# Kernel optimization log

Hardware: AMD Instinct MI355X
Metric: run time of the kernel (lower is better)

The kernel has to match this reference:

```python
import jax, jax.numpy as jnp
import numpy as np

EPS = 1e-12  # matches torch.nn.functional.normalize default eps


def _l2norm_ch(x):
    # normalize over channel axis (dim=1), x: [B, D, N]
    n = jnp.sqrt(jnp.sum(x * x, axis=1, keepdims=True))
    return x / jnp.maximum(n, EPS)


def setup_inputs() -> dict:
    key = jax.random.key(0)
    k0, k1, kq, kk, kv = jax.random.split(key, 5)
    B, D, H, W = 8, 128, 64, 64
    return {
        "vol0": jax.random.normal(k0, (B, D, H, W), dtype=jnp.float32),
        "vol1": jax.random.normal(k1, (B, D, H, W), dtype=jnp.float32),
        "Wq": jax.random.normal(kq, (D, D), dtype=jnp.float32) * 0.05,
        "Wk": jax.random.normal(kk, (D, D), dtype=jnp.float32) * 0.05,
        "Wv": jax.random.normal(kv, (D, D), dtype=jnp.float32) * 0.05,
    }


def reference(vol0, vol1, Wq, Wk, Wv):
    B, D, H, W = vol0.shape
    N = H * W
    x0 = vol0.reshape(B, D, N)
    x1 = vol1.reshape(B, D, N)

    # 1x1 convs (bias=False) == channel matmuls; residual connections enabled
    q = jnp.einsum('od,bdn->bon', Wq, x0) + x0
    k = jnp.einsum('od,bdn->bon', Wk, x1) + x1
    v0 = jnp.einsum('od,bdn->bon', Wv, x0) + x0
    v1 = jnp.einsum('od,bdn->bon', Wv, x1) + x1

    # normalise dot product: L2-normalize over channel dim
    q = _l2norm_ch(q)
    k = _l2norm_ch(k)

    # correlation volume + row softmax: cvolume[b, n, m]
    cvolume = jax.nn.softmax(jnp.einsum('bdn,bdm->bnm', q, k), axis=2)

    # warp v1 by attention: v1w[b, d, n] = sum_m v1[b, d, m] * cvolume[b, n, m]
    v1w = jnp.einsum('bdm,bnm->bdn', v1, cvolume)

    # position encoder (meshgrid with 'ij' indexing, as legacy torch.meshgrid)
    u = jnp.linspace(-1.0, 1.0, H)
    v = jnp.linspace(-1.0, 1.0, W)
    uu, vv = jnp.meshgrid(u, v, indexing='ij')
    grid = jnp.stack([uu, vv], axis=0).reshape(2, N)  # [2, N]
    pos = jnp.einsum('cm,bnm->bcn', grid, cvolume)  # [B, 2, N]

    # max-score channel: [B, 1, N]
    max_score = jnp.max(cvolume, axis=2)[:, None, :]

    agg = jnp.concatenate([v0, v1w, pos, max_score], axis=1)  # [B, 2D+3, N]
    return agg.reshape(B, 2 * D + 3, H, W)
```

## Files before the change

kernel.cpp:

```cpp
#include <hip/hip_runtime.h>
#include <hip/hip_bf16.h>

#define B_   8
#define D_   128
#define N_   4096
#define CH   259

typedef short bf8 __attribute__((ext_vector_type(8)));
typedef float f4  __attribute__((ext_vector_type(4)));

typedef unsigned int as1_u32 __attribute__((address_space(1)));
typedef unsigned int as3_u32 __attribute__((address_space(3)));

__device__ __forceinline__ void gll16(const void* g, void* l) {
    __builtin_amdgcn_global_load_lds((as1_u32*)(unsigned long long)g,
                                     (as3_u32*)(unsigned int)(unsigned long long)l,
                                     16, 0, 0);
}

__device__ __forceinline__ unsigned short f2bf(float x) {
    unsigned int u = __float_as_uint(x);
    return (unsigned short)((u + 0x7FFFu + ((u >> 16) & 1u)) >> 16);
}

__device__ __forceinline__ unsigned int cvtpk(float lo, float hi) {
    unsigned int r;
    asm("v_cvt_pk_bf16_f32 %0, %1, %2" : "=v"(r) : "v"(lo), "v"(hi));
    return r;
}

__global__ void wconv_kernel(const float* __restrict__ Wq,
                             const float* __restrict__ Wk,
                             const float* __restrict__ Wv,
                             unsigned short* __restrict__ Wb) {
    const float* src = (blockIdx.x == 0) ? Wq : (blockIdx.x == 1) ? Wk : Wv;
    unsigned short* dst = Wb + (size_t)blockIdx.x * D_ * D_;
    for (int i = threadIdx.x; i < D_ * D_; i += blockDim.x) dst[i] = f2bf(src[i]);
}

__global__ __launch_bounds__(256, 2) void proj_kernel(
    const float* __restrict__ vol0, const float* __restrict__ vol1,
    const unsigned short* __restrict__ Wb, float* __restrict__ out,
    unsigned short* __restrict__ Qp, unsigned short* __restrict__ Kh,
    unsigned short* __restrict__ V1T)
{
    __shared__ __align__(16) float xs[2][D_ * 64];

    const int tid  = threadIdx.x;
    const int wave = tid >> 6, lane = tid & 63;
    const int l15  = lane & 15, lh = lane >> 4;

    const int bid = blockIdx.x;
    const int swz = (bid & 7) * 64 + (bid >> 3);
    const int b   = swz >> 6;
    const int n0  = (swz & 63) * 64;

    #pragma unroll
    for (int a = 0; a < 2; ++a) {
        const char* src = (const char*)((a ? vol1 : vol0) + (size_t)b * D_ * N_ + n0);
        char* dstb = (char*)&xs[a][0];
        #pragma unroll
        for (int i = 0; i < 8; ++i) {
            int dst16 = i * 4096 + tid * 16;
            int row = dst16 >> 8, cb = dst16 & 255;
            gll16(src + (size_t)row * (N_ * 4) + (cb ^ (((row >> 3) & 7) << 4)), dstb + dst16);
        }
    }
    __syncthreads();

    const int nrow = wave * 16 + l15;

    auto afrag = [&](const float* base, int k) -> bf8 {
        const int dbase = k * 32 + lh * 8;
        const unsigned int cb = ((unsigned int)(nrow * 4)) ^ (((unsigned int)((k * 4 + lh) & 7)) << 4);
        const float* p = base + dbase * 64 + (cb >> 2);
        union { bf8 v; unsigned int w[4]; } u;
        #pragma unroll
        for (int jj = 0; jj < 4; ++jj)
            u.w[jj] = cvtpk(p[(2 * jj) * 64], p[(2 * jj + 1) * 64]);
        return u.v;
    };

    f4 aq[8], ak[8], a0v[8], a1v[8];
    #pragma unroll
    for (int ob = 0; ob < 8; ++ob) {
        aq[ob] = (f4){0.f,0.f,0.f,0.f}; ak[ob] = (f4){0.f,0.f,0.f,0.f};
        a0v[ob] = (f4){0.f,0.f,0.f,0.f}; a1v[ob] = (f4){0.f,0.f,0.f,0.f};
    }

    const unsigned short* Wqb = Wb;
    const unsigned short* Wkb = Wb + D_ * D_;
    const unsigned short* Wvb = Wb + 2 * D_ * D_;

    for (int k = 0; k < 4; ++k) {
        bf8 x0f = afrag(&xs[0][0], k);
        bf8 x1f = afrag(&xs[1][0], k);
        #pragma unroll
        for (int ob = 0; ob < 8; ++ob) {
            const size_t woff = ((size_t)(ob * 16 + l15)) * D_ + k * 32 + lh * 8;
            bf8 wq = *(const bf8*)(Wqb + woff);
            bf8 wk = *(const bf8*)(Wkb + woff);
            bf8 wv = *(const bf8*)(Wvb + woff);
            aq[ob]  = __builtin_amdgcn_mfma_f32_16x16x32_bf16(x0f, wq, aq[ob], 0, 0, 0);
            ak[ob]  = __builtin_amdgcn_mfma_f32_16x16x32_bf16(x1f, wk, ak[ob], 0, 0, 0);
            a0v[ob] = __builtin_amdgcn_mfma_f32_16x16x32_bf16(x0f, wv, a0v[ob], 0, 0, 0);
            a1v[ob] = __builtin_amdgcn_mfma_f32_16x16x32_bf16(x1f, wv, a1v[ob], 0, 0, 0);
        }
    }

    float ssq[4] = {0.f,0.f,0.f,0.f}, ssk[4] = {0.f,0.f,0.f,0.f};
    #pragma unroll
    for (int ob = 0; ob < 8; ++ob) {
        const int o = ob * 16 + l15;
        const unsigned int okey = (((unsigned int)((o >> 3) & 7)) << 4);
        #pragma unroll
        for (int r = 0; r < 4; ++r) {
            int n = wave * 16 + lh * 4 + r;
            int ci = o * 64 + (int)(((((unsigned int)(n * 4)) ^ okey) >> 2));
            float r0 = xs[0][ci], r1 = xs[1][ci];
            aq[ob][r] += r0; ak[ob][r] += r1; a0v[ob][r] += r0; a1v[ob][r] += r1;
            ssq[r] = fmaf(aq[ob][r], aq[ob][r], ssq[r]);
            ssk[r] = fmaf(ak[ob][r], ak[ob][r], ssk[r]);
        }
    }
    #pragma unroll
    for (int off = 1; off < 16; off <<= 1)
        #pragma unroll
        for (int r = 0; r < 4; ++r) {
            ssq[r] += __shfl_xor(ssq[r], off, 64);
            ssk[r] += __shfl_xor(ssk[r], off, 64);
        }
    float rq[4], rk[4];
    #pragma unroll
    for (int r = 0; r < 4; ++r) {
        rq[r] = 1.44269504088896f / fmaxf(sqrtf(ssq[r]), 1e-12f);
        rk[r] = 1.0f / fmaxf(sqrtf(ssk[r]), 1e-12f);
    }

    const int nbase = n0 + wave * 16 + lh * 4;
    #pragma unroll
    for (int ob = 0; ob < 8; ++ob) {
        const int o = ob * 16 + l15;
        *(f4*)(out + ((size_t)(b * CH + o)) * N_ + nbase) = a0v[ob];
        uint2 pv; pv.x = cvtpk(a1v[ob][0], a1v[ob][1]); pv.y = cvtpk(a1v[ob][2], a1v[ob][3]);
        *(uint2*)(V1T + ((size_t)(b * D_ + o)) * N_ + nbase) = pv;
        uint2 pq; pq.x = cvtpk(aq[ob][0]*rq[0], aq[ob][1]*rq[1]);
        pq.y = cvtpk(aq[ob][2]*rq[2], aq[ob][3]*rq[3]);
        *(uint2*)(Qp + ((size_t)(b * D_ + o)) * N_ + nbase) = pq;
    }

    __syncthreads();
    float* chunk = &xs[0][0] + wave * 2176;
    #pragma unroll
    for (int ob = 0; ob < 8; ++ob) {
        const int o = ob * 16 + l15;
        #pragma unroll
        for (int r = 0; r < 4; ++r) chunk[o * 17 + lh * 4 + r] = ak[ob][r] * rk[r];
    }
    asm volatile("s_waitcnt lgkmcnt(0)" ::: "memory");
    __builtin_amdgcn_sched_barrier(0);
    {
        const int o0 = (lane & 15) * 8, nr = lane >> 4;
        #pragma unroll
        for (int t = 0; t < 4; ++t) {
            int nl = t * 4 + nr;
            float f[8];
            #pragma unroll
            for (int j = 0; j < 8; ++j) f[j] = chunk[(o0 + j) * 17 + nl];
            uint4 st;
            st.x = cvtpk(f[0], f[1]); st.y = cvtpk(f[2], f[3]);
            st.z = cvtpk(f[4], f[5]); st.w = cvtpk(f[6], f[7]);
            *(uint4*)(Kh + ((size_t)(b * N_ + n0 + wave * 16 + nl)) * D_ + o0) = st;
        }
    }
}

__global__ __launch_bounds__(256, 2) void attn_kernel(
    const unsigned short* __restrict__ Qp, const unsigned short* __restrict__ Kh,
    const unsigned short* __restrict__ V1T, float* __restrict__ out)
{
    __shared__ __align__(16) char smem[73728];
    char* KB = smem;
    char* VB = smem + 32768;
    char* PB = smem + 65536;

    const int tid  = threadIdx.x;
    const int wave = tid >> 6, lane = tid & 63;
    const int l15  = lane & 15, lh = lane >> 4;
    const int mhalf = wave & 1, qpair = wave >> 1;

    const int bid = blockIdx.x;
    const int swz = (bid & 7) * 64 + (bid >> 3);
    const int b   = swz >> 6;
    const int n0  = (swz & 63) * 64;
    const int nw  = n0 + qpair * 32;

    bf8 qf[2][4];
    const unsigned short* Qb = Qp + (size_t)b * D_ * N_;
    #pragma unroll
    for (int qg = 0; qg < 2; ++qg)
        #pragma unroll
        for (int dc = 0; dc < 4; ++dc) {
            union { bf8 v; unsigned short e[8]; } u;
            #pragma unroll
            for (int j = 0; j < 8; ++j)
                u.e[j] = Qb[((size_t)(dc * 32 + lh * 8 + j)) * N_ + nw + qg * 16 + l15];
            qf[qg][dc] = u.v;
        }

    f4 acc[2][8];
    #pragma unroll
    for (int qg = 0; qg < 2; ++qg)
        #pragma unroll
        for (int dc = 0; dc < 8; ++dc) acc[qg][dc] = (f4){0.f,0.f,0.f,0.f};
    float lsum[2] = {0.f, 0.f}, pu[2] = {0.f, 0.f}, pvv[2] = {0.f, 0.f};
    float Mp[2] = {-1e30f, -1e30f};

    float vb0[8];
    #pragma unroll
    for (int s = 0; s < 2; ++s)
        #pragma unroll
        for (int r = 0; r < 4; ++r)
            vb0[s * 4 + r] = -1.f + (2.f / 63.f) * (float)(s * 16 + lh * 4 + r);

    const char* Kbytes = (const char*)(Kh + (size_t)b * N_ * D_);
    const char* Vbytes = (const char*)(V1T + (size_t)b * D_ * N_);
    char* Pw = PB + wave * 2048;

    unsigned int koffs[4], voffs[4];
    #pragma unroll
    for (int ii = 0; ii < 4; ++ii) {
        int r = wave * 16 + ii * 4 + (lane >> 4);
        unsigned int col = (unsigned int)((lane & 15) * 16);
        koffs[ii] = (unsigned int)(((r >> 5) * 2048 + (r & 31)) * 256)
                  + (col ^ (unsigned int)((r & 7) << 4));
        int vr = wave * 64 + ii * 16 + (lane >> 2);
        int ch = vr & 127;
        unsigned int mc = (unsigned int)((lane & 3) * 16);
        voffs[ii] = (unsigned int)(ch * 8192 + (vr >> 7) * 4096)
                  + (mc ^ (unsigned int)(((ch >> 1) & 3) << 4));
    }
    auto stage = [&](int buf, int t) {
        const char* ks = Kbytes + (size_t)t * 8192;
        char* kd = KB + buf * 16384 + wave * 4096;
        #pragma unroll
        for (int ii = 0; ii < 4; ++ii) gll16(ks + koffs[ii], kd + ii * 1024);
        const char* vs = Vbytes + (size_t)t * 64;
        char* vd = VB + buf * 16384 + wave * 4096;
        #pragma unroll
        for (int ii = 0; ii < 4; ++ii) gll16(vs + voffs[ii], vd + ii * 1024);
    };

    unsigned int kcol[4];
    #pragma unroll
    for (int dc = 0; dc < 4; ++dc)
        kcol[dc] = ((unsigned int)(dc * 64 + lh * 16)) ^ ((unsigned int)((l15 & 7) << 4));
    const unsigned int pkey  = ((unsigned int)((l15 >> 1) & 3)) << 4;
    const unsigned int prow0 = (unsigned int)(l15 * 64);
    const unsigned int prow1 = (unsigned int)((16 + l15) * 64);
    const unsigned int vx    = ((unsigned int)(lh * 16)) ^ pkey;

    stage(0, 0);
    __syncthreads();

    const float utb = -1.f + (2.f / 63.f) * (float)(mhalf * 32);

    for (int t = 0; t < 64; ++t) {
        const int cur = t & 1;
        if (t + 1 < 64) stage(cur ^ 1, t + 1);

        const char* Kc = KB + cur * 16384 + mhalf * 8192 + l15 * 256;
        const char* Vc = VB + cur * 16384 + mhalf * 8192 + l15 * 64;

        f4 s00 = (f4){0.f,0.f,0.f,0.f}, s01 = (f4){0.f,0.f,0.f,0.f};
        f4 s10 = (f4){0.f,0.f,0.f,0.f}, s11 = (f4){0.f,0.f,0.f,0.f};
        __builtin_amdgcn_s_setprio(1);
        #pragma unroll
        for (int dc = 0; dc < 4; ++dc) {
            bf8 k0 = *(const bf8*)(Kc + kcol[dc]);
            bf8 k1 = *(const bf8*)(Kc + 4096 + kcol[dc]);
            s00 = __builtin_amdgcn_mfma_f32_16x16x32_bf16(k0, qf[0][dc], s00, 0, 0, 0);
            s10 = __builtin_amdgcn_mfma_f32_16x16x32_bf16(k0, qf[1][dc], s10, 0, 0, 0);
            s01 = __builtin_amdgcn_mfma_f32_16x16x32_bf16(k1, qf[0][dc], s01, 0, 0, 0);
            s11 = __builtin_amdgcn_mfma_f32_16x16x32_bf16(k1, qf[1][dc], s11, 0, 0, 0);
        }
        __builtin_amdgcn_s_setprio(0);

        const float ut   = utb + (2.f / 63.f) * (float)(t >> 1);
        const float voff = (t & 1) ? (64.f / 63.f) : 0.f;
        #pragma unroll
        for (int qg = 0; qg < 2; ++qg) {
            f4 sa = qg ? s10 : s00, sb = qg ? s11 : s01;
            float p[8];
            #pragma unroll
            for (int r = 0; r < 4; ++r) {
                p[r]     = __builtin_amdgcn_exp2f(sa[r]);
                p[4 + r] = __builtin_amdgcn_exp2f(sb[r]);
            }
            Mp[qg] = fmaxf(Mp[qg], fmaxf(fmaxf(fmaxf(sa[0], sa[1]), fmaxf(sa[2], sa[3])),
                                         fmaxf(fmaxf(sb[0], sb[1]), fmaxf(sb[2], sb[3]))));
            float ps = ((p[0]+p[1]) + (p[2]+p[3])) + ((p[4]+p[5]) + (p[6]+p[7]));
            float pvp = 0.f;
            #pragma unroll
            for (int i = 0; i < 8; ++i) pvp = fmaf(vb0[i], p[i], pvp);
            lsum[qg] += ps;
            pu[qg]  = fmaf(ut, ps, pu[qg]);
            pvv[qg] = fmaf(voff, ps, pvv[qg] + pvp);
            const unsigned int pr = qg ? prow1 : prow0;
            uint2 w0; w0.x = cvtpk(p[0], p[1]); w0.y = cvtpk(p[2], p[3]);
            uint2 w1; w1.x = cvtpk(p[4], p[5]); w1.y = cvtpk(p[6], p[7]);
            *(uint2*)(Pw + pr + (((unsigned int)(lh * 8)) ^ pkey))      = w0;
            *(uint2*)(Pw + pr + (((unsigned int)(32 + lh * 8)) ^ pkey)) = w1;
        }
        asm volatile("s_waitcnt lgkmcnt(0)" ::: "memory");
        __builtin_amdgcn_sched_barrier(0);

        bf8 pf0 = *(const bf8*)(Pw + prow0 + vx);
        bf8 pf1 = *(const bf8*)(Pw + prow1 + vx);
        __builtin_amdgcn_s_setprio(1);
        #pragma unroll
        for (int dc = 0; dc < 8; ++dc) {
            bf8 vf = *(const bf8*)(Vc + dc * 1024 + vx);
            acc[0][dc] = __builtin_amdgcn_mfma_f32_16x16x32_bf16(pf0, vf, acc[0][dc], 0, 0, 0);
            acc[1][dc] = __builtin_amdgcn_mfma_f32_16x16x32_bf16(pf1, vf, acc[1][dc], 0, 0, 0);
        }
        __builtin_amdgcn_s_setprio(0);
        __syncthreads();
    }

    #pragma unroll
    for (int qg = 0; qg < 2; ++qg) {
        #pragma unroll
        for (int off = 16; off < 64; off <<= 1) {
            lsum[qg] += __shfl_xor(lsum[qg], off, 64);
            pu[qg]   += __shfl_xor(pu[qg], off, 64);
            pvv[qg]  += __shfl_xor(pvv[qg], off, 64);
            Mp[qg]    = fmaxf(Mp[qg], __shfl_xor(Mp[qg], off, 64));
        }
    }

    __syncthreads();
    float* ex  = (float*)smem;
    float* stt = (float*)(smem + 34816);
    if (lane < 16) {
        #pragma unroll
        for (int qg = 0; qg < 2; ++qg) {
            float* s = stt + ((wave * 2 + qg) * 16 + l15) * 4;
            s[0] = lsum[qg]; s[1] = pu[qg]; s[2] = pvv[qg]; s[3] = Mp[qg];
        }
    }
    #pragma unroll
    for (int qg = 0; qg < 2; ++qg)
        #pragma unroll
        for (int j = 0; j < 4; ++j) {
            float* e = ex + (((wave * 2 + qg) * 4 + j) * 16 + lh * 4) * 17 + l15;
            if (mhalf == 0) {
                #pragma unroll
                for (int r = 0; r < 4; ++r) e[r * 17] = acc[qg][4 + j][r];
            } else {
                #pragma unroll
                for (int r = 0; r < 4; ++r) e[r * 17] = acc[qg][j][r];
            }
        }
    __syncthreads();

    const int pw_ = wave ^ 1;
    float rl[2], PUm[2], PVm[2], Mm[2];
    #pragma unroll
    for (int qg = 0; qg < 2; ++qg) {
        const float* s = stt + ((pw_ * 2 + qg) * 16 + l15) * 4;
        float Lm = lsum[qg] + s[0];
        PUm[qg] = pu[qg]  + s[1];
        PVm[qg] = pvv[qg] + s[2];
        Mm[qg]  = fmaxf(Mp[qg], s[3]);
        rl[qg]  = __builtin_amdgcn_rcpf(Lm);
    }

    #pragma unroll
    for (int qg = 0; qg < 2; ++qg) {
        float rlr[4];
        #pragma unroll
        for (int r = 0; r < 4; ++r)
            rlr[r] = __shfl(rl[qg], (lane & 48) + lh * 4 + r, 64);
        #pragma unroll
        for (int j = 0; j < 4; ++j) {
            const float* e = ex + (((pw_ * 2 + qg) * 4 + j) * 16 + lh * 4) * 17 + l15;
            f4 v;
            if (mhalf == 0) {
                #pragma unroll
                for (int r = 0; r < 4; ++r) v[r] = (acc[qg][j][r] + e[r * 17]) * rlr[r];
            } else {
                #pragma unroll
                for (int r = 0; r < 4; ++r) v[r] = (acc[qg][4 + j][r] + e[r * 17]) * rlr[r];
            }
            const int och = 128 + (mhalf * 4 + j) * 16 + l15;
            *(f4*)(out + ((size_t)(b * CH + och)) * N_ + nw + qg * 16 + lh * 4) = v;
        }
    }
    if (mhalf == 0 && lh == 0) {
        #pragma unroll
        for (int qg = 0; qg < 2; ++qg) {
            const int gn = nw + qg * 16 + l15;
            out[((size_t)(b * CH + 256)) * N_ + gn] = PUm[qg] * rl[qg];
            out[((size_t)(b * CH + 257)) * N_ + gn] = PVm[qg] * rl[qg];
            out[((size_t)(b * CH + 258)) * N_ + gn] =
                __builtin_amdgcn_exp2f(Mm[qg]) * rl[qg];
        }
    }
}

extern "C" void kernel_launch(void* const* d_in, const int* in_sizes, int n_in,
                              void* d_out, int out_size, void* d_ws, size_t ws_size,
                              hipStream_t stream) {
    const float* vol0 = (const float*)d_in[0];
    const float* vol1 = (const float*)d_in[1];
    const float* Wq   = (const float*)d_in[2];
    const float* Wk   = (const float*)d_in[3];
    const float* Wv   = (const float*)d_in[4];
    float* out = (float*)d_out;

    char* ws = (char*)d_ws;
    const size_t QP_BYTES  = (size_t)B_ * D_ * N_ * 2;
    const size_t KH_BYTES  = (size_t)B_ * N_ * D_ * 2;
    const size_t V1T_BYTES = (size_t)B_ * D_ * N_ * 2;
    unsigned short* Qp  = (unsigned short*)(ws);
    unsigned short* Kh  = (unsigned short*)(ws + QP_BYTES);
    unsigned short* V1T = (unsigned short*)(ws + QP_BYTES + KH_BYTES);
    unsigned short* Wb  = (unsigned short*)(ws + QP_BYTES + KH_BYTES + V1T_BYTES);

    hipLaunchKernelGGL(wconv_kernel, dim3(3), dim3(256), 0, stream, Wq, Wk, Wv, Wb);
    hipLaunchKernelGGL(proj_kernel, dim3(512), dim3(256), 0, stream,
                       vol0, vol1, Wb, out, Qp, Kh, V1T);
    hipLaunchKernelGGL(attn_kernel, dim3(512), dim3(256), 0, stream,
                       Qp, Kh, V1T, out);
}
```

Measured before the change: 152.1 us.

## Load V fragments directly from global memory in a tiled layout, dropping the V LDS stage

The projection kernel now writes V1 in a chunked layout, so each attention wave can fetch its MFMA B-operand fragments for V straight from global memory as contiguous 16-byte loads. The V double buffer in LDS is removed, shrinking shared memory from 72KB to 40KB, and launch bounds are raised to allow 3 blocks per CU. The aim is less LDS traffic and higher occupancy. In exchange, global load latency is exposed inside the loop, since the loads are issued at the start of each iteration, and 8 bf8 fragments per iteration add register pressure.

```diff
diff --git a/kernel.cpp b/kernel.cpp
--- a/kernel.cpp
+++ b/kernel.cpp
@@ -42,7 +42,7 @@
     const float* __restrict__ vol0, const float* __restrict__ vol1,
     const unsigned short* __restrict__ Wb, float* __restrict__ out,
     unsigned short* __restrict__ Qp, unsigned short* __restrict__ Kh,
-    unsigned short* __restrict__ V1T)
+    unsigned short* __restrict__ V2)
 {
     __shared__ __align__(16) float xs[2][D_ * 64];
 
@@ -138,12 +138,17 @@
     }
 
     const int nbase = n0 + wave * 16 + lh * 4;
+    const int mh_ = nbase >> 11;
+    const int tt  = (nbase & 2047) >> 5;
+    const int ml  = nbase & 31;
+    char* v2chunk = (char*)V2 + (((size_t)(b * 2 + mh_) * 64 + tt) * 8192) + ml * 2;
+
     #pragma unroll
     for (int ob = 0; ob < 8; ++ob) {
         const int o = ob * 16 + l15;
         *(f4*)(out + ((size_t)(b * CH + o)) * N_ + nbase) = a0v[ob];
         uint2 pv; pv.x = cvtpk(a1v[ob][0], a1v[ob][1]); pv.y = cvtpk(a1v[ob][2], a1v[ob][3]);
-        *(uint2*)(V1T + ((size_t)(b * D_ + o)) * N_ + nbase) = pv;
+        *(uint2*)(v2chunk + (size_t)o * 64) = pv;
         uint2 pq; pq.x = cvtpk(aq[ob][0]*rq[0], aq[ob][1]*rq[1]);
         pq.y = cvtpk(aq[ob][2]*rq[2], aq[ob][3]*rq[3]);
         *(uint2*)(Qp + ((size_t)(b * D_ + o)) * N_ + nbase) = pq;
@@ -175,14 +180,13 @@
     }
 }
 
-__global__ __launch_bounds__(256, 2) void attn_kernel(
+__global__ __launch_bounds__(256, 3) void attn_kernel(
     const unsigned short* __restrict__ Qp, const unsigned short* __restrict__ Kh,
-    const unsigned short* __restrict__ V1T, float* __restrict__ out)
+    const unsigned short* __restrict__ V2, float* __restrict__ out)
 {
-    __shared__ __align__(16) char smem[73728];
+    __shared__ __align__(16) char smem[40960];
     char* KB = smem;
-    char* VB = smem + 32768;
-    char* PB = smem + 65536;
+    char* PB = smem + 32768;
 
     const int tid  = threadIdx.x;
     const int wave = tid >> 6, lane = tid & 63;
@@ -224,31 +228,23 @@
             vb0[s * 4 + r] = -1.f + (2.f / 63.f) * (float)(s * 16 + lh * 4 + r);
 
     const char* Kbytes = (const char*)(Kh + (size_t)b * N_ * D_);
-    const char* Vbytes = (const char*)(V1T + (size_t)b * D_ * N_);
+    const char* Vg = (const char*)V2 + ((size_t)(b * 2 + mhalf)) * 524288
+                   + l15 * 64 + lh * 16;
     char* Pw = PB + wave * 2048;
 
-    unsigned int koffs[4], voffs[4];
+    unsigned int koffs[4];
     #pragma unroll
     for (int ii = 0; ii < 4; ++ii) {
         int r = wave * 16 + ii * 4 + (lane >> 4);
         unsigned int col = (unsigned int)((lane & 15) * 16);
         koffs[ii] = (unsigned int)(((r >> 5) * 2048 + (r & 31)) * 256)
                   + (col ^ (unsigned int)((r & 7) << 4));
-        int vr = wave * 64 + ii * 16 + (lane >> 2);
-        int ch = vr & 127;
-        unsigned int mc = (unsigned int)((lane & 3) * 16);
-        voffs[ii] = (unsigned int)(ch * 8192 + (vr >> 7) * 4096)
-                  + (mc ^ (unsigned int)(((ch >> 1) & 3) << 4));
     }
     auto stage = [&](int buf, int t) {
         const char* ks = Kbytes + (size_t)t * 8192;
         char* kd = KB + buf * 16384 + wave * 4096;
         #pragma unroll
         for (int ii = 0; ii < 4; ++ii) gll16(ks + koffs[ii], kd + ii * 1024);
-        const char* vs = Vbytes + (size_t)t * 64;
-        char* vd = VB + buf * 16384 + wave * 4096;
-        #pragma unroll
-        for (int ii = 0; ii < 4; ++ii) gll16(vs + voffs[ii], vd + ii * 1024);
     };
 
     unsigned int kcol[4];
@@ -258,7 +254,7 @@
     const unsigned int pkey  = ((unsigned int)((l15 >> 1) & 3)) << 4;
     const unsigned int prow0 = (unsigned int)(l15 * 64);
     const unsigned int prow1 = (unsigned int)((16 + l15) * 64);
-    const unsigned int vx    = ((unsigned int)(lh * 16)) ^ pkey;
+    const unsigned int px    = ((unsigned int)(lh * 16)) ^ pkey;
 
     stage(0, 0);
     __syncthreads();
@@ -267,10 +263,15 @@
 
     for (int t = 0; t < 64; ++t) {
         const int cur = t & 1;
+
+        const char* vp = Vg + t * 8192;
+        bf8 vf[8];
+        #pragma unroll
+        for (int dc = 0; dc < 8; ++dc) vf[dc] = *(const bf8*)(vp + dc * 1024);
+
         if (t + 1 < 64) stage(cur ^ 1, t + 1);
 
         const char* Kc = KB + cur * 16384 + mhalf * 8192 + l15 * 256;
-        const char* Vc = VB + cur * 16384 + mhalf * 8192 + l15 * 64;
 
         f4 s00 = (f4){0.f,0.f,0.f,0.f}, s01 = (f4){0.f,0.f,0.f,0.f};
         f4 s10 = (f4){0.f,0.f,0.f,0.f}, s11 = (f4){0.f,0.f,0.f,0.f};
@@ -315,14 +316,13 @@
         asm volatile("s_waitcnt lgkmcnt(0)" ::: "memory");
         __builtin_amdgcn_sched_barrier(0);
 
-        bf8 pf0 = *(const bf8*)(Pw + prow0 + vx);
-        bf8 pf1 = *(const bf8*)(Pw + prow1 + vx);
+        bf8 pf0 = *(const bf8*)(Pw + prow0 + px);
+        bf8 pf1 = *(const bf8*)(Pw + prow1 + px);
         __builtin_amdgcn_s_setprio(1);
         #pragma unroll
         for (int dc = 0; dc < 8; ++dc) {
-            bf8 vf = *(const bf8*)(Vc + dc * 1024 + vx);
-            acc[0][dc] = __builtin_amdgcn_mfma_f32_16x16x32_bf16(pf0, vf, acc[0][dc], 0, 0, 0);
-            acc[1][dc] = __builtin_amdgcn_mfma_f32_16x16x32_bf16(pf1, vf, acc[1][dc], 0, 0, 0);
+            acc[0][dc] = __builtin_amdgcn_mfma_f32_16x16x32_bf16(pf0, vf[dc], acc[0][dc], 0, 0, 0);
+            acc[1][dc] = __builtin_amdgcn_mfma_f32_16x16x32_bf16(pf1, vf[dc], acc[1][dc], 0, 0, 0);
         }
         __builtin_amdgcn_s_setprio(0);
         __syncthreads();
@@ -422,15 +422,15 @@
     char* ws = (char*)d_ws;
     const size_t QP_BYTES  = (size_t)B_ * D_ * N_ * 2;
     const size_t KH_BYTES  = (size_t)B_ * N_ * D_ * 2;
-    const size_t V1T_BYTES = (size_t)B_ * D_ * N_ * 2;
+    const size_t V2_BYTES  = (size_t)B_ * D_ * N_ * 2;
     unsigned short* Qp  = (unsigned short*)(ws);
     unsigned short* Kh  = (unsigned short*)(ws + QP_BYTES);
-    unsigned short* V1T = (unsigned short*)(ws + QP_BYTES + KH_BYTES);
-    unsigned short* Wb  = (unsigned short*)(ws + QP_BYTES + KH_BYTES + V1T_BYTES);
+    unsigned short* V2  = (unsigned short*)(ws + QP_BYTES + KH_BYTES);
+    unsigned short* Wb  = (unsigned short*)(ws + QP_BYTES + KH_BYTES + V2_BYTES);
 
     hipLaunchKernelGGL(wconv_kernel, dim3(3), dim3(256), 0, stream, Wq, Wk, Wv, Wb);
     hipLaunchKernelGGL(proj_kernel, dim3(512), dim3(256), 0, stream,
-                       vol0, vol1, Wb, out, Qp, Kh, V1T);
+                       vol0, vol1, Wb, out, Qp, Kh, V2);
     hipLaunchKernelGGL(attn_kernel, dim3(512), dim3(256), 0, stream,
-                       Qp, Kh, V1T, out);
-}
+                       Qp, Kh, V2, out);
+}
```

Measured after the change: 312.6 us. +105.6%, slower.
